# Kernel optimization log

Measured on AMD Instinct MI355X. Metric: run time of the kernel, lower is better.

## Reference

```python
import jax, jax.numpy as jnp
import numpy as np
import math

B, L, CH, H, NL, N2 = 32, 4096, 1, 256, 4, 32  # batch, seq, channels, d_model, n_layers, d_state//2
LN_EPS = 1e-5


def setup_inputs() -> dict:
    key = jax.random.key(0)
    ks = jax.random.split(key, 12)
    rn = lambda k, shape, s=1.0: (jax.random.normal(k, shape, dtype=jnp.float32) * s)
    inp = {}
    inp["x"] = rn(ks[0], (B, L, CH))
    inp["enc_w"] = rn(ks[1], (H, CH), 1.0 / math.sqrt(CH))
    inp["enc_b"] = jnp.zeros((H,), jnp.float32)
    # S4D kernel parameters, stacked over layers (standard S4D init)
    dt_min, dt_max = 1e-3, 1e-1
    u = jax.random.uniform(ks[2], (NL, H))
    inp["log_dt"] = (u * (math.log(dt_max) - math.log(dt_min)) + math.log(dt_min)).astype(jnp.float32)
    inp["log_A_real"] = jnp.full((NL, H, N2), math.log(0.5), jnp.float32)
    inp["A_imag"] = jnp.broadcast_to(math.pi * jnp.arange(N2, dtype=jnp.float32), (NL, H, N2)) + jnp.zeros((NL, H, N2), jnp.float32)
    inp["C_re"] = rn(ks[3], (NL, H, N2))
    inp["C_im"] = rn(ks[4], (NL, H, N2))
    inp["D"] = rn(ks[5], (NL, H))
    # output_linear: 1x1 Conv1d H->2H followed by GLU
    inp["glu_w"] = rn(ks[6], (NL, 2 * H, H), 1.0 / math.sqrt(H))
    inp["glu_b"] = jnp.zeros((NL, 2 * H), jnp.float32)
    inp["ln_g"] = jnp.ones((NL, H), jnp.float32)
    inp["ln_b"] = jnp.zeros((NL, H), jnp.float32)
    inp["dec1_w"] = rn(ks[7], (1, L), 1.0 / math.sqrt(L))
    inp["dec1_b"] = jnp.zeros((1,), jnp.float32)
    inp["dec2_w"] = rn(ks[8], (1, H), 1.0 / math.sqrt(H))
    inp["dec2_b"] = jnp.zeros((1,), jnp.float32)
    return inp


def _s4d_layer(u_bhl, log_dt, log_A_real, A_imag, C_re, C_im, D, glu_w, glu_b):
    """S4D block on (B, H, L): FFT conv with diagonal-SSM kernel + skip D + GELU + GLU output linear."""
    Lx = u_bhl.shape[-1]
    dt = jnp.exp(log_dt)                          # (H,)
    A = -jnp.exp(log_A_real) + 1j * A_imag        # (H, N2) complex
    C = C_re + 1j * C_im                          # (H, N2)
    dtA = A * dt[:, None]                         # (H, N2)
    Ck = C * (jnp.exp(dtA) - 1.0) / A             # ZOH-style discretized C
    # Vandermonde kernel: k[h, l] = 2 * Re( sum_n Ck[h,n] * exp(dtA[h,n] * l) )
    expdtA = jnp.exp(dtA[:, :, None] * jnp.arange(Lx, dtype=jnp.float32))  # (H, N2, L)
    k = 2.0 * jnp.einsum('hn,hnl->hl', Ck, expdtA).real                    # (H, L)
    # causal conv via zero-padded FFT
    kf = jnp.fft.rfft(k, n=2 * Lx)
    uf = jnp.fft.rfft(u_bhl, n=2 * Lx)
    y = jnp.fft.irfft(uf * kf, n=2 * Lx)[..., :Lx]
    y = y + u_bhl * D[:, None]
    y = jax.nn.gelu(y, approximate=False)
    # 1x1 conv H -> 2H, then GLU over the channel dim
    y = jnp.einsum('oh,bhl->bol', glu_w, y) + glu_b[:, None]
    a, g = jnp.split(y, 2, axis=-2)
    return a * jax.nn.sigmoid(g)


def reference(x, enc_w, enc_b, log_dt, log_A_real, A_imag, C_re, C_im, D,
              glu_w, glu_b, ln_g, ln_b, dec1_w, dec1_b, dec2_w, dec2_b):
    h = x @ enc_w.T + enc_b                 # (B, L, H)
    h = jnp.swapaxes(h, -1, -2)             # (B, H, L)
    for i in range(NL):
        z = _s4d_layer(h, log_dt[i], log_A_real[i], A_imag[i], C_re[i], C_im[i],
                       D[i], glu_w[i], glu_b[i])
        h = z + h                           # residual (dropout = identity in eval)
        ht = jnp.swapaxes(h, -1, -2)        # (B, L, H) -> LayerNorm over H (postnorm)
        mu = ht.mean(-1, keepdims=True)
        var = ht.var(-1, keepdims=True)
        ht = (ht - mu) / jnp.sqrt(var + LN_EPS) * ln_g[i] + ln_b[i]
        h = jnp.swapaxes(ht, -1, -2)
    y = jnp.einsum('bhl,ol->bho', h, dec1_w) + dec1_b   # (B, H, 1)
    y = y.squeeze(-1)                                    # (B, H)
    y = y @ dec2_w.T + dec2_b                            # (B, 1)
    y = y.squeeze(-1)                                    # (B,)
    return jax.nn.sigmoid(y)
```

## Files before the change

kernel.cpp:

```cpp
#include <hip/hip_runtime.h>
#include <math.h>

#define WS_WT   16777216
#define WS_Y1   17039360
#define WS_A256 17047552
#define WS_V    17063936
#define WS_ABUF 19161088
#define WS_S    29646848

typedef unsigned short ushort_t;
struct __attribute__((aligned(8))) us4 { ushort_t x, y, z, w; };
typedef short bf16x8 __attribute__((ext_vector_type(8)));
typedef float f32x4  __attribute__((ext_vector_type(4)));

__device__ __forceinline__ float bf2f(ushort_t u) {
    union { unsigned int i; float f; } c; c.i = ((unsigned int)u) << 16; return c.f;
}
__device__ __forceinline__ ushort_t f2bf(float f) {
    union { float f; unsigned int i; } c; c.f = f;
    unsigned int x = c.i;
    unsigned int r = (x + 0x7FFF + ((x >> 16) & 1)) >> 16;
    return (ushort_t)r;
}
__device__ __forceinline__ float fast_gelu(float v) {
    float y = 1.5957691216057308f * (v + 0.044715f * v * v * v);
    return v / (1.f + __expf(-y));
}

__global__ __launch_bounds__(256) void enc_kernel(const float* __restrict__ x,
    const float* __restrict__ ew, const float* __restrict__ eb, ushort_t* __restrict__ Hb)
{
    int i = blockIdx.x * 256 + threadIdx.x;
    int l8 = i & 511;
    int h  = (i >> 9) & 255;
    int b  = i >> 17;
    const float* xp = x + ((size_t)b << 12) + (l8 << 3);
    float4 a0 = ((const float4*)xp)[0];
    float4 a1 = ((const float4*)xp)[1];
    float w = ew[h], bb = eb[h];
    us4 o0, o1;
    o0.x = f2bf(fmaf(a0.x, w, bb)); o0.y = f2bf(fmaf(a0.y, w, bb));
    o0.z = f2bf(fmaf(a0.z, w, bb)); o0.w = f2bf(fmaf(a0.w, w, bb));
    o1.x = f2bf(fmaf(a1.x, w, bb)); o1.y = f2bf(fmaf(a1.y, w, bb));
    o1.z = f2bf(fmaf(a1.z, w, bb)); o1.w = f2bf(fmaf(a1.w, w, bb));
    us4* op = (us4*)(Hb + ((size_t)i << 3));
    op[0] = o0; op[1] = o1;
}

__global__ __launch_bounds__(256) void wtb_kernel(const float* __restrict__ gw, ushort_t* __restrict__ wTb)
{
    int i = blockIdx.x * 256 + threadIdx.x;
    wTb[i] = f2bf(gw[i]);
}

__global__ __launch_bounds__(256) void prep_kernel(
    const float* __restrict__ log_dt, const float* __restrict__ lAr,
    const float* __restrict__ Aim_, const float* __restrict__ Cre,
    const float* __restrict__ Cim, ushort_t* __restrict__ Abuf,
    ushort_t* __restrict__ Vg, float* __restrict__ a256tab, int li)
{
    __shared__ float s_ar[32], s_ai[32], s_ckr[32], s_cki[32];
    __shared__ float powr[8][32], powi[8][32];
    __shared__ float karr[256];
    __shared__ ushort_t Vt[256][66];
    int t = threadIdx.x;
    int h = blockIdx.x;
    int pb = (li * 256 + h) * 32;

    if (t < 32) {
        int s = t;
        float dt = expf(log_dt[li * 256 + h]);
        float Are = -expf(lAr[pb + s]);
        float Ai  = Aim_[pb + s];
        float e = expf(Are * dt);
        float ar = e * cosf(Ai * dt), ai = e * sinf(Ai * dt);
        float inv = 1.f / (Are * Are + Ai * Ai);
        float numr = ar - 1.f, numi = ai;
        float tr = (numr * Are + numi * Ai) * inv;
        float ti = (numi * Are - numr * Ai) * inv;
        float cr = Cre[pb + s], ci = Cim[pb + s];
        s_ar[s] = ar; s_ai[s] = ai;
        s_ckr[s] = 2.f * (cr * tr - ci * ti);
        s_cki[s] = 2.f * (cr * ti + ci * tr);
        float xr = ar, xi = ai;
        for (int k = 0; k < 8; k++) {
            powr[k][s] = xr; powi[k][s] = xi;
            float nr = xr * xr - xi * xi;
            float ni = 2.f * xr * xi;
            xr = nr; xi = ni;
        }
        a256tab[h * 64 + s * 2] = xr;
        a256tab[h * 64 + s * 2 + 1] = xi;
    }
    __syncthreads();

    int d = t;
    float adr[32], adi[32];
    #pragma unroll
    for (int s = 0; s < 32; s++) { adr[s] = 1.f; adi[s] = 0.f; }
    #pragma unroll
    for (int bit = 0; bit < 8; bit++) {
        if (d & (1 << bit)) {
            #pragma unroll
            for (int s = 0; s < 32; s++) {
                float pr_ = powr[bit][s], pi_ = powi[bit][s];
                float nr = adr[s] * pr_ - adi[s] * pi_;
                float ni = adr[s] * pi_ + adi[s] * pr_;
                adr[s] = nr; adi[s] = ni;
            }
        }
    }
    float kd = 0.f;
    #pragma unroll
    for (int s = 0; s < 32; s++) kd += s_ckr[s] * adr[s] - s_cki[s] * adi[s];
    karr[d] = kd;
    unsigned int wrow[32];
    #pragma unroll
    for (int s = 0; s < 32; s++) {
        float wr = adr[s] * s_ar[s] - adi[s] * s_ai[s];
        float wi = adr[s] * s_ai[s] + adi[s] * s_ar[s];
        float v0 = s_ckr[s] * wr - s_cki[s] * wi;
        float v1 = -(s_ckr[s] * wi + s_cki[s] * wr);
        wrow[s] = (unsigned int)f2bf(v0) | ((unsigned int)f2bf(v1) << 16);
    }
    {
        ushort_t* arow = Abuf + (size_t)h * 81920 + (size_t)d * 320 + 256;
        #pragma unroll
        for (int q = 0; q < 8; q++) {
            uint4 v; v.x = wrow[q*4]; v.y = wrow[q*4+1]; v.z = wrow[q*4+2]; v.w = wrow[q*4+3];
            *(uint4*)(arow + q * 8) = v;
        }
    }
    {
        int e = 255 - d;
        float evr[32], evi[32];
        #pragma unroll
        for (int s = 0; s < 32; s++) { evr[s] = 1.f; evi[s] = 0.f; }
        #pragma unroll
        for (int bit = 0; bit < 8; bit++) {
            if (e & (1 << bit)) {
                #pragma unroll
                for (int s = 0; s < 32; s++) {
                    float pr_ = powr[bit][s], pi_ = powi[bit][s];
                    float nr = evr[s] * pr_ - evi[s] * pi_;
                    float ni = evr[s] * pi_ + evi[s] * pr_;
                    evr[s] = nr; evi[s] = ni;
                }
            }
        }
        #pragma unroll
        for (int s = 0; s < 32; s++) {
            Vt[d][2*s]   = f2bf(evr[s]);
            Vt[d][2*s+1] = f2bf(evi[s]);
        }
    }
    __syncthreads();

    {
        ushort_t* trow = Abuf + (size_t)h * 81920 + (size_t)t * 320;
        for (int j4 = 0; j4 < 64; j4++) {
            int j = j4 * 4;
            us4 v;
            v.x = (j     <= t) ? f2bf(karr[t - j    ]) : (ushort_t)0;
            v.y = (j + 1 <= t) ? f2bf(karr[t - j - 1]) : (ushort_t)0;
            v.z = (j + 2 <= t) ? f2bf(karr[t - j - 2]) : (ushort_t)0;
            v.w = (j + 3 <= t) ? f2bf(karr[t - j - 3]) : (ushort_t)0;
            *(us4*)(trow + j) = v;
        }
    }
    {
        int m = t >> 2, jq = t & 3;
        ushort_t* vrow = Vg + (size_t)h * 16384 + (size_t)m * 256 + jq * 64;
        for (int j4 = 0; j4 < 16; j4++) {
            int j = jq * 64 + j4 * 4;
            us4 v;
            v.x = Vt[j][m]; v.y = Vt[j+1][m]; v.z = Vt[j+2][m]; v.w = Vt[j+3][m];
            *(us4*)(vrow + j4 * 4) = v;
        }
    }
}

__global__ __launch_bounds__(256, 2) void s4df_kernel(
    const ushort_t* __restrict__ U, const ushort_t* __restrict__ Abuf,
    const ushort_t* __restrict__ Vg, const float* __restrict__ a256tab,
    const float* __restrict__ Dp, ushort_t* __restrict__ G, int li, int b0)
{
    __shared__ ushort_t yt[64 * 320];
    __shared__ ushort_t sS[64 * 66];
    int t = threadIdx.x;
    int h = blockIdx.x;
    int tile = blockIdx.y;
    int nl = t & 63, kq = t >> 6;
    int n = tile * 64 + nl;
    int sw = nl & 7;
    const ushort_t* ub = U + (size_t)(b0 + (n >> 4)) * 1048576 + (size_t)h * 4096 + (n & 15) * 256;
    #pragma unroll
    for (int i = 0; i < 8; i++) {
        int c = kq * 8 + i;
        *(uint4*)(&yt[nl * 320 + ((c ^ sw) << 3)]) = *(const uint4*)(ub + c * 8);
    }
    __syncthreads();

    int lane = t & 63, w = t >> 6;
    int ln15 = lane & 15, quad = lane >> 4;
    int rsw = ln15 & 7;

    {
        const ushort_t* va = Vg + (size_t)h * 16384 + (size_t)(w * 16 + ln15) * 256;
        f32x4 acc[4] = {};
        for (int ks = 0; ks < 8; ks++) {
            int c = ks * 4 + quad;
            bf16x8 af = *(const bf16x8*)(va + ks * 32 + quad * 8);
            #pragma unroll
            for (int nt = 0; nt < 4; nt++) {
                bf16x8 bf_ = *(const bf16x8*)(&yt[(nt * 16 + ln15) * 320 + ((c ^ rsw) << 3)]);
                acc[nt] = __builtin_amdgcn_mfma_f32_16x16x32_bf16(af, bf_, acc[nt], 0, 0, 0);
            }
        }
        #pragma unroll
        for (int nt = 0; nt < 4; nt++) {
            int m = w * 16 + quad * 4;
            int nn = nt * 16 + ln15;
            sS[(m    ) * 66 + nn] = f2bf(acc[nt][0]);
            sS[(m + 1) * 66 + nn] = f2bf(acc[nt][1]);
            sS[(m + 2) * 66 + nn] = f2bf(acc[nt][2]);
            sS[(m + 3) * 66 + nn] = f2bf(acc[nt][3]);
        }
    }
    __syncthreads();

    if (t < 128) {
        int bq = t >> 5, s = t & 31;
        float m2r = a256tab[h * 64 + s * 2], m2i = a256tab[h * 64 + s * 2 + 1];
        int col = 256 + 2 * s;
        int cc = col >> 3, off = col & 7;
        float sr = 0.f, si = 0.f;
        for (int c = 0; c < 16; c++) {
            int nn = bq * 16 + c;
            float Sr = bf2f(sS[(2 * s) * 66 + nn]);
            float Si = bf2f(sS[(2 * s + 1) * 66 + nn]);
            int addr = nn * 320 + ((cc ^ (nn & 7)) << 3) + off;
            yt[addr] = f2bf(sr);
            yt[addr + 1] = f2bf(si);
            float nsr = m2r * sr - m2i * si + Sr;
            float nsi = m2r * si + m2i * sr + Si;
            sr = nsr; si = nsi;
        }
    }
    __syncthreads();

    const ushort_t* Ah = Abuf + (size_t)h * 81920;
    f32x4 acc[4][4] = {};
    for (int ks = 0; ks < 10; ks++) {
        int kk = ks * 32 + quad * 8;
        int c = ks * 4 + quad;
        bf16x8 af[4];
        #pragma unroll
        for (int mt = 0; mt < 4; mt++)
            af[mt] = *(const bf16x8*)(Ah + (size_t)(w * 64 + mt * 16 + ln15) * 320 + kk);
        #pragma unroll
        for (int nt = 0; nt < 4; nt++) {
            bf16x8 bf_ = *(const bf16x8*)(&yt[(nt * 16 + ln15) * 320 + ((c ^ rsw) << 3)]);
            #pragma unroll
            for (int mt = 0; mt < 4; mt++)
                acc[mt][nt] = __builtin_amdgcn_mfma_f32_16x16x32_bf16(af[mt], bf_, acc[mt][nt], 0, 0, 0);
        }
    }
    float Dh = Dp[li * 256 + h];
    #pragma unroll
    for (int mt = 0; mt < 4; mt++) {
        #pragma unroll
        for (int nt = 0; nt < 4; nt++) {
            int nn = tile * 64 + nt * 16 + ln15;
            int lb = w * 64 + mt * 16 + quad * 4;
            int c = lb >> 3, co = lb & 7;
            us4 uv = *(const us4*)(&yt[(nt * 16 + ln15) * 320 + ((c ^ rsw) << 3) + co]);
            float uu[4] = {bf2f(uv.x), bf2f(uv.y), bf2f(uv.z), bf2f(uv.w)};
            us4 o;
            ushort_t* op = &o.x;
            #pragma unroll
            for (int rr = 0; rr < 4; rr++) {
                float v = acc[mt][nt][rr] + Dh * uu[rr];
                op[rr] = f2bf(fast_gelu(v));
            }
            ushort_t* gp = G + ((size_t)(nn >> 4) * 256 + h) * 4096 + (nn & 15) * 256 + lb;
            *(us4*)gp = o;
        }
    }
}

#define LDK 268
__global__ __launch_bounds__(256, 2) void gluln_kernel(
    const ushort_t* __restrict__ G, const ushort_t* __restrict__ wTb,
    const float* __restrict__ glu_b, const float* __restrict__ ln_g,
    const float* __restrict__ ln_b, ushort_t* __restrict__ Hb, int li, int b0)
{
    __shared__ ushort_t yt[64 * LDK];
    __shared__ float sred[4][64], sqred[4][64];
    __shared__ float mup[64], rstd[64];
    int t = threadIdx.x;
    int pf = blockIdx.x * 64;
    int bloc = pf >> 12;
    int l0 = pf & 4095;
    int b = b0 + bloc;

    const ushort_t* gb = G + (size_t)bloc * 1048576 + l0;
    unsigned int* dst = (unsigned int*)&yt[0];
    #pragma unroll
    for (int i = 0; i < 4; i++) {
        int hp = ((i & 1) << 6) + (t >> 2);
        int pg = ((i >> 1) << 2) + (t & 3);
        int h0 = hp * 2;
        uint4 va = *(const uint4*)(gb + (size_t)h0 * 4096 + pg * 8);
        uint4 vb = *(const uint4*)(gb + (size_t)(h0 + 1) * 4096 + pg * 8);
        const ushort_t* ra = (const ushort_t*)&va;
        const ushort_t* rb = (const ushort_t*)&vb;
        #pragma unroll
        for (int j = 0; j < 8; j++) {
            unsigned int v = (unsigned int)ra[j] | ((unsigned int)rb[j] << 16);
            dst[(pg * 8 + j) * (LDK / 2) + hp] = v;
        }
    }
    __syncthreads();

    int lane = t & 63, w = t >> 6;
    int ln15 = lane & 15, quad = lane >> 4;
    int oA = w * 64;
    const ushort_t* wA = wTb + li * 131072;

    f32x4 accA[4][4] = {};
    f32x4 accG[4][4] = {};

    for (int ks = 0; ks < 8; ks++) {
        int kk = ks * 32 + quad * 8;
        bf16x8 af[4], gf[4];
        #pragma unroll
        for (int mt = 0; mt < 4; mt++) {
            int oa = oA + mt * 16 + ln15;
            af[mt] = *(const bf16x8*)(wA + (size_t)oa * 256 + kk);
            gf[mt] = *(const bf16x8*)(wA + (size_t)(oa + 256) * 256 + kk);
        }
        bf16x8 bfr[4];
        #pragma unroll
        for (int nt = 0; nt < 4; nt++) {
            const us4* yp = (const us4*)&yt[(nt * 16 + ln15) * LDK + kk];
            us4 lo = yp[0], hi = yp[1];
            bf16x8 v;
            v[0] = (short)lo.x; v[1] = (short)lo.y; v[2] = (short)lo.z; v[3] = (short)lo.w;
            v[4] = (short)hi.x; v[5] = (short)hi.y; v[6] = (short)hi.z; v[7] = (short)hi.w;
            bfr[nt] = v;
        }
        #pragma unroll
        for (int mt = 0; mt < 4; mt++)
            #pragma unroll
            for (int nt = 0; nt < 4; nt++) {
                accA[mt][nt] = __builtin_amdgcn_mfma_f32_16x16x32_bf16(bfr[nt], af[mt], accA[mt][nt], 0, 0, 0);
                accG[mt][nt] = __builtin_amdgcn_mfma_f32_16x16x32_bf16(bfr[nt], gf[mt], accG[mt][nt], 0, 0, 0);
            }
    }

    ushort_t* hb_ = Hb + (size_t)b * 1048576;
    us4 hold[4][4];
    #pragma unroll
    for (int mt = 0; mt < 4; mt++) {
        const ushort_t* hrow = hb_ + (size_t)(oA + mt * 16 + ln15) * 4096 + l0 + quad * 4;
        #pragma unroll
        for (int nt = 0; nt < 4; nt++)
            hold[mt][nt] = *(const us4*)(hrow + nt * 16);
    }

    float ba[4], bg[4];
    #pragma unroll
    for (int mt = 0; mt < 4; mt++) {
        int o = oA + mt * 16 + ln15;
        ba[mt] = glu_b[li * 512 + o];
        bg[mt] = glu_b[li * 512 + 256 + o];
    }

    float psl[4][4] = {}, pql[4][4] = {};
    #pragma unroll
    for (int mt = 0; mt < 4; mt++) {
        #pragma unroll
        for (int nt = 0; nt < 4; nt++) {
            const ushort_t* hp4 = &hold[mt][nt].x;
            #pragma unroll
            for (int r = 0; r < 4; r++) {
                float a = accA[mt][nt][r] + ba[mt];
                float g = accG[mt][nt][r] + bg[mt];
                float z = a / (1.f + __expf(-g));
                float hn = z + bf2f(hp4[r]);
                accA[mt][nt][r] = hn;
                psl[nt][r] += hn; pql[nt][r] = fmaf(hn, hn, pql[nt][r]);
            }
        }
    }
    #pragma unroll
    for (int nt = 0; nt < 4; nt++)
        #pragma unroll
        for (int r = 0; r < 4; r++) {
            float s = psl[nt][r], q = pql[nt][r];
            s += __shfl_xor(s, 1, 64); q += __shfl_xor(q, 1, 64);
            s += __shfl_xor(s, 2, 64); q += __shfl_xor(q, 2, 64);
            s += __shfl_xor(s, 4, 64); q += __shfl_xor(q, 4, 64);
            s += __shfl_xor(s, 8, 64); q += __shfl_xor(q, 8, 64);
            psl[nt][r] = s; pql[nt][r] = q;
        }
    if (ln15 == 0) {
        #pragma unroll
        for (int nt = 0; nt < 4; nt++)
            #pragma unroll
            for (int r = 0; r < 4; r++) {
                int p = nt * 16 + quad * 4 + r;
                sred[w][p] = psl[nt][r];
                sqred[w][p] = pql[nt][r];
            }
    }
    __syncthreads();
    if (t < 64) {
        float S = (sred[0][t] + sred[1][t]) + (sred[2][t] + sred[3][t]);
        float Q = (sqred[0][t] + sqred[1][t]) + (sqred[2][t] + sqred[3][t]);
        float mu = S * (1.f / 256.f);
        float var = Q * (1.f / 256.f) - mu * mu;
        mup[t] = mu; rstd[t] = rsqrtf(var + 1e-5f);
    }
    __syncthreads();

    #pragma unroll
    for (int mt = 0; mt < 4; mt++) {
        int o = oA + mt * 16 + ln15;
        float gm = ln_g[li * 256 + o];
        float bt = ln_b[li * 256 + o];
        ushort_t* hrow = hb_ + (size_t)o * 4096 + l0 + quad * 4;
        #pragma unroll
        for (int nt = 0; nt < 4; nt++) {
            us4 ov;
            ushort_t* op = &ov.x;
            #pragma unroll
            for (int r = 0; r < 4; r++) {
                int p = nt * 16 + quad * 4 + r;
                float v = (accA[mt][nt][r] - mup[p]) * rstd[p] * gm + bt;
                op[r] = f2bf(v);
            }
            *(us4*)(hrow + nt * 16) = ov;
        }
    }
}

__global__ __launch_bounds__(256) void dec1_kernel(const ushort_t* __restrict__ Hb,
    const float* __restrict__ w1, const float* __restrict__ b1, float* __restrict__ y1)
{
    int bh = blockIdx.x;
    const ushort_t* base = Hb + (size_t)bh * 4096;
    int t = threadIdx.x;
    float s = 0.f;
    for (int l = t; l < 4096; l += 256) s = fmaf(bf2f(base[l]), w1[l], s);
    #pragma unroll
    for (int d = 32; d > 0; d >>= 1) s += __shfl_xor(s, d, 64);
    __shared__ float red[4];
    if ((t & 63) == 0) red[t >> 6] = s;
    __syncthreads();
    if (t == 0) y1[bh] = red[0] + red[1] + red[2] + red[3] + b1[0];
}

__global__ __launch_bounds__(256) void dec2_kernel(const float* __restrict__ y1,
    const float* __restrict__ w2, const float* __restrict__ b2, float* __restrict__ out)
{
    int t = threadIdx.x;
    int b = blockIdx.x * 4 + (t >> 6);
    int lane = t & 63;
    float s = 0.f;
    #pragma unroll
    for (int k = 0; k < 4; k++) s = fmaf(y1[b * 256 + lane + k * 64], w2[lane + k * 64], s);
    #pragma unroll
    for (int d = 32; d > 0; d >>= 1) s += __shfl_xor(s, d, 64);
    if (lane == 0) out[b] = 1.f / (1.f + expf(-(s + b2[0])));
}

extern "C" void kernel_launch(void* const* d_in, const int* in_sizes, int n_in,
                              void* d_out, int out_size, void* d_ws, size_t ws_size,
                              hipStream_t stream)
{
    const float* x      = (const float*)d_in[0];
    const float* enc_w  = (const float*)d_in[1];
    const float* enc_b  = (const float*)d_in[2];
    const float* log_dt = (const float*)d_in[3];
    const float* lAr    = (const float*)d_in[4];
    const float* Aim    = (const float*)d_in[5];
    const float* Cre    = (const float*)d_in[6];
    const float* Cim    = (const float*)d_in[7];
    const float* Dp     = (const float*)d_in[8];
    const float* glu_w  = (const float*)d_in[9];
    const float* glu_b  = (const float*)d_in[10];
    const float* ln_g   = (const float*)d_in[11];
    const float* ln_b   = (const float*)d_in[12];
    const float* w1     = (const float*)d_in[13];
    const float* b1     = (const float*)d_in[14];
    const float* w2     = (const float*)d_in[15];
    const float* b2     = (const float*)d_in[16];

    float* ws = (float*)d_ws;
    ushort_t* Hb   = (ushort_t*)ws;
    ushort_t* wTb  = (ushort_t*)(ws + WS_WT);
    float* y1      = ws + WS_Y1;
    float* a256    = ws + WS_A256;
    ushort_t* Vg   = (ushort_t*)(ws + WS_V);
    ushort_t* Abuf = (ushort_t*)(ws + WS_ABUF);
    float* outp    = (float*)d_out;

    size_t wsf = ws_size / 4;
    int nb = 32;
    while (nb > 4 && (size_t)WS_S + (size_t)nb * 655360 > wsf) nb >>= 1;
    ushort_t* Gb = (ushort_t*)(ws + WS_S + (size_t)nb * 131072);

    wtb_kernel<<<2048, 256, 0, stream>>>(glu_w, wTb);
    enc_kernel<<<16384, 256, 0, stream>>>(x, enc_w, enc_b, Hb);
    for (int li = 0; li < 4; li++) {
        prep_kernel<<<256, 256, 0, stream>>>(log_dt, lAr, Aim, Cre, Cim, Abuf, Vg, a256, li);
        for (int b0 = 0; b0 < 32; b0 += nb) {
            s4df_kernel<<<dim3(256, nb / 4), 256, 0, stream>>>(Hb, Abuf, Vg, a256, Dp, Gb, li, b0);
            gluln_kernel<<<nb * 64, 256, 0, stream>>>(Gb, wTb, glu_b, ln_g, ln_b, Hb, li, b0);
        }
    }
    dec1_kernel<<<8192, 256, 0, stream>>>(Hb, w1, b1, y1);
    dec2_kernel<<<8, 256, 0, stream>>>(y1, w2, b2, outp);
}
```

Measured before the change: 1.019 ms.

## Restructure GLU+LayerNorm kernel per M-tile to cut registers and raise occupancy

The GLU GEMM in the fused GLU/LayerNorm kernel now runs one 16-row output tile at a time. It computes the gate and value accumulators in turn, applies the GLU and residual, and stores the pre-norm values packed as bf16 in registers instead of holding 32 fp32 accumulator tiles. This lowers register pressure so launch bounds can target 3 blocks per SM instead of 2. The trade-offs are that the activation tile is re-read from LDS for each M-tile, which raises LDS traffic about 8x, and the pre-norm value is rounded to bf16 before normalisation.

```diff
diff --git a/kernel.cpp b/kernel.cpp
--- a/kernel.cpp
+++ b/kernel.cpp
@@ -15,6 +15,12 @@
 
 __device__ __forceinline__ float bf2f(ushort_t u) {
     union { unsigned int i; float f; } c; c.i = ((unsigned int)u) << 16; return c.f;
+}
+__device__ __forceinline__ float bf2f_lo(unsigned int u) {
+    union { unsigned int i; float f; } c; c.i = u << 16; return c.f;
+}
+__device__ __forceinline__ float bf2f_hi(unsigned int u) {
+    union { unsigned int i; float f; } c; c.i = u & 0xFFFF0000u; return c.f;
 }
 __device__ __forceinline__ ushort_t f2bf(float f) {
     union { float f; unsigned int i; } c; c.f = f;
@@ -290,7 +296,7 @@
 }
 
 #define LDK 268
-__global__ __launch_bounds__(256, 2) void gluln_kernel(
+__global__ __launch_bounds__(256, 3) void gluln_kernel(
     const ushort_t* __restrict__ G, const ushort_t* __restrict__ wTb,
     const float* __restrict__ glu_b, const float* __restrict__ ln_g,
     const float* __restrict__ ln_b, ushort_t* __restrict__ Hb, int li, int b0)
@@ -327,73 +333,68 @@
     int ln15 = lane & 15, quad = lane >> 4;
     int oA = w * 64;
     const ushort_t* wA = wTb + li * 131072;
-
-    f32x4 accA[4][4] = {};
-    f32x4 accG[4][4] = {};
-
-    for (int ks = 0; ks < 8; ks++) {
-        int kk = ks * 32 + quad * 8;
-        bf16x8 af[4], gf[4];
-        #pragma unroll
-        for (int mt = 0; mt < 4; mt++) {
-            int oa = oA + mt * 16 + ln15;
-            af[mt] = *(const bf16x8*)(wA + (size_t)oa * 256 + kk);
-            gf[mt] = *(const bf16x8*)(wA + (size_t)(oa + 256) * 256 + kk);
-        }
-        bf16x8 bfr[4];
-        #pragma unroll
-        for (int nt = 0; nt < 4; nt++) {
-            const us4* yp = (const us4*)&yt[(nt * 16 + ln15) * LDK + kk];
-            us4 lo = yp[0], hi = yp[1];
-            bf16x8 v;
-            v[0] = (short)lo.x; v[1] = (short)lo.y; v[2] = (short)lo.z; v[3] = (short)lo.w;
-            v[4] = (short)hi.x; v[5] = (short)hi.y; v[6] = (short)hi.z; v[7] = (short)hi.w;
-            bfr[nt] = v;
-        }
-        #pragma unroll
-        for (int mt = 0; mt < 4; mt++)
-            #pragma unroll
-            for (int nt = 0; nt < 4; nt++) {
-                accA[mt][nt] = __builtin_amdgcn_mfma_f32_16x16x32_bf16(bfr[nt], af[mt], accA[mt][nt], 0, 0, 0);
-                accG[mt][nt] = __builtin_amdgcn_mfma_f32_16x16x32_bf16(bfr[nt], gf[mt], accG[mt][nt], 0, 0, 0);
-            }
-    }
-
     ushort_t* hb_ = Hb + (size_t)b * 1048576;
-    us4 hold[4][4];
-    #pragma unroll
-    for (int mt = 0; mt < 4; mt++) {
-        const ushort_t* hrow = hb_ + (size_t)(oA + mt * 16 + ln15) * 4096 + l0 + quad * 4;
-        #pragma unroll
-        for (int nt = 0; nt < 4; nt++)
-            hold[mt][nt] = *(const us4*)(hrow + nt * 16);
-    }
-
-    float ba[4], bg[4];
+
+    unsigned int hn2[4][4][2];
+    float psl[4][4] = {}, pql[4][4] = {};
+
     #pragma unroll
     for (int mt = 0; mt < 4; mt++) {
         int o = oA + mt * 16 + ln15;
-        ba[mt] = glu_b[li * 512 + o];
-        bg[mt] = glu_b[li * 512 + 256 + o];
-    }
-
-    float psl[4][4] = {}, pql[4][4] = {};
-    #pragma unroll
-    for (int mt = 0; mt < 4; mt++) {
+        us4 hold[4];
+        const ushort_t* hrow = hb_ + (size_t)o * 4096 + l0 + quad * 4;
+        #pragma unroll
+        for (int nt = 0; nt < 4; nt++) hold[nt] = *(const us4*)(hrow + nt * 16);
+        float bav = glu_b[li * 512 + o];
+        float bgv = glu_b[li * 512 + 256 + o];
+        const ushort_t* wgp = wA + (size_t)(o + 256) * 256;
+        const ushort_t* wap = wA + (size_t)o * 256;
+
+        f32x4 accG[4] = {};
+        for (int ks = 0; ks < 8; ks++) {
+            int kk = ks * 32 + quad * 8;
+            bf16x8 gf = *(const bf16x8*)(wgp + kk);
+            #pragma unroll
+            for (int nt = 0; nt < 4; nt++) {
+                const us4* yp = (const us4*)&yt[(nt * 16 + ln15) * LDK + kk];
+                us4 lo = yp[0], hi = yp[1];
+                bf16x8 v;
+                v[0] = (short)lo.x; v[1] = (short)lo.y; v[2] = (short)lo.z; v[3] = (short)lo.w;
+                v[4] = (short)hi.x; v[5] = (short)hi.y; v[6] = (short)hi.z; v[7] = (short)hi.w;
+                accG[nt] = __builtin_amdgcn_mfma_f32_16x16x32_bf16(v, gf, accG[nt], 0, 0, 0);
+            }
+        }
+        f32x4 accA[4] = {};
+        for (int ks = 0; ks < 8; ks++) {
+            int kk = ks * 32 + quad * 8;
+            bf16x8 af = *(const bf16x8*)(wap + kk);
+            #pragma unroll
+            for (int nt = 0; nt < 4; nt++) {
+                const us4* yp = (const us4*)&yt[(nt * 16 + ln15) * LDK + kk];
+                us4 lo = yp[0], hi = yp[1];
+                bf16x8 v;
+                v[0] = (short)lo.x; v[1] = (short)lo.y; v[2] = (short)lo.z; v[3] = (short)lo.w;
+                v[4] = (short)hi.x; v[5] = (short)hi.y; v[6] = (short)hi.z; v[7] = (short)hi.w;
+                accA[nt] = __builtin_amdgcn_mfma_f32_16x16x32_bf16(v, af, accA[nt], 0, 0, 0);
+            }
+        }
         #pragma unroll
         for (int nt = 0; nt < 4; nt++) {
-            const ushort_t* hp4 = &hold[mt][nt].x;
+            const ushort_t* hp4 = &hold[nt].x;
+            float hv[4];
             #pragma unroll
             for (int r = 0; r < 4; r++) {
-                float a = accA[mt][nt][r] + ba[mt];
-                float g = accG[mt][nt][r] + bg[mt];
-                float z = a / (1.f + __expf(-g));
+                float sig = 1.f / (1.f + __expf(-(accG[nt][r] + bgv)));
+                float z = (accA[nt][r] + bav) * sig;
                 float hn = z + bf2f(hp4[r]);
-                accA[mt][nt][r] = hn;
+                hv[r] = hn;
                 psl[nt][r] += hn; pql[nt][r] = fmaf(hn, hn, pql[nt][r]);
             }
-        }
-    }
+            hn2[mt][nt][0] = (unsigned int)f2bf(hv[0]) | ((unsigned int)f2bf(hv[1]) << 16);
+            hn2[mt][nt][1] = (unsigned int)f2bf(hv[2]) | ((unsigned int)f2bf(hv[3]) << 16);
+        }
+    }
+
     #pragma unroll
     for (int nt = 0; nt < 4; nt++)
         #pragma unroll
@@ -433,12 +434,15 @@
         ushort_t* hrow = hb_ + (size_t)o * 4096 + l0 + quad * 4;
         #pragma unroll
         for (int nt = 0; nt < 4; nt++) {
+            float hv[4];
+            hv[0] = bf2f_lo(hn2[mt][nt][0]); hv[1] = bf2f_hi(hn2[mt][nt][0]);
+            hv[2] = bf2f_lo(hn2[mt][nt][1]); hv[3] = bf2f_hi(hn2[mt][nt][1]);
             us4 ov;
             ushort_t* op = &ov.x;
             #pragma unroll
             for (int r = 0; r < 4; r++) {
                 int p = nt * 16 + quad * 4 + r;
-                float v = (accA[mt][nt][r] - mup[p]) * rstd[p] * gm + bt;
+                float v = (hv[r] - mup[p]) * rstd[p] * gm + bt;
                 op[r] = f2bf(v);
             }
             *(us4*)(hrow + nt * 16) = ov;
```

Measured after the change: 1.256 ms. +23.3%, slower.
